# Kernel tuning notes

Measured on AMD Instinct MI355X. Metric: run time of the kernel, lower is better.

The kernel has to match this reference:

```python
import jax, jax.numpy as jnp
from jax import lax
import numpy as np

B, T, F = 64, 128, 16
H = 512
S = 2  # num_seg; SEG_DICT['2'] = [8, 6], seg_cumsum = [2, 10, 16]


def timestep_embedding(t, dim, max_period=10000.0):
    half = dim // 2
    freqs = jnp.exp(-jnp.log(max_period) * jnp.arange(half, dtype=jnp.float32) / half)
    args = t[:, None] * freqs  # [N, half]
    return jnp.concatenate([jnp.cos(args), jnp.sin(args)], axis=-1)  # [N, dim]


def setup_inputs() -> dict:
    key = jax.random.key(0)
    ks = jax.random.split(key, 16)
    sc = lambda *sh: 1.0 / np.sqrt(sh[-1])
    inp = {
        'x': jax.random.normal(ks[0], (B, T, F), dtype=jnp.float32),
        'lengths': jax.random.randint(ks[1], (B,), 1, T + 1),
        'h0': jax.random.uniform(ks[2], (B, H), dtype=jnp.float32),
        'c0': jax.random.uniform(ks[3], (B, H), dtype=jnp.float32),
        'W_is0': jax.random.normal(ks[4], (H, 8), dtype=jnp.float32) * sc(8),
        'b_is0': jax.random.normal(ks[5], (H,), dtype=jnp.float32) * 0.01,
        'W_is1': jax.random.normal(ks[6], (H, 6), dtype=jnp.float32) * sc(6),
        'b_is1': jax.random.normal(ks[7], (H,), dtype=jnp.float32) * 0.01,
        'W_ih': jax.random.normal(ks[8], (4 * H, 3 * H), dtype=jnp.float32) * sc(3 * H),
        'W_hh': jax.random.normal(ks[9], (4 * H, H), dtype=jnp.float32) * sc(H),
        'b_ih': jax.random.normal(ks[10], (4 * H,), dtype=jnp.float32) * 0.01,
        'b_hh': jax.random.normal(ks[11], (4 * H,), dtype=jnp.float32) * 0.01,
        'W_o': jax.random.normal(ks[12], (F - 2, S * H), dtype=jnp.float32) * sc(S * H),
        'b_o': jax.random.normal(ks[13], (F - 2,), dtype=jnp.float32) * 0.01,
    }
    return inp


def reference(x, lengths, h0, c0, W_is0, b_is0, W_is1, b_is1,
              W_ih, W_hh, b_ih, b_hh, W_o, b_o):
    b, t, f = x.shape
    h = h0.shape[1]
    xf = x.reshape(-1, f)  # [B*T, F]

    # timestep embeddings from the two time columns (learning_type='diff')
    tc = timestep_embedding(xf[:, 0], h)
    tp = timestep_embedding(xf[:, 1], h)
    t_emb = jnp.concatenate([tc, tp], axis=-1)  # [B*T, 2H]

    # per-segment input linears (segments = cols 2:10 and 10:16)
    e0 = xf[:, 2:10] @ W_is0.T + b_is0
    e1 = xf[:, 10:16] @ W_is1.T + b_is1
    e0 = jnp.concatenate([e0, t_emb], axis=-1)[:, None, :]  # [B*T, 1, 3H]
    e1 = jnp.concatenate([e1, t_emb], axis=-1)[:, None, :]
    # faithful to torch: concat on dim=1 then reshape(batch, num_seg, seq_len, -1)
    embs = jnp.concatenate([e0, e1], axis=1).reshape(b, S, t, 3 * h)

    def cell(carry, xt):
        hh, cc = carry
        gates = xt @ W_ih.T + b_ih + hh @ W_hh.T + b_hh
        i, fg, g, o = jnp.split(gates, 4, axis=-1)  # torch LSTMCell order i,f,g,o
        cc = jax.nn.sigmoid(fg) * cc + jax.nn.sigmoid(i) * jnp.tanh(g)
        hh = jax.nn.sigmoid(o) * jnp.tanh(cc)
        return (hh, cc), hh

    hs = []
    for s in range(S):  # shared cell weights across segments (same nn.LSTMCell object)
        xs = jnp.swapaxes(embs[:, s], 0, 1)  # [T, B, 3H]
        _, h_seq = lax.scan(cell, (h0, c0), xs)  # [T, B, H]
        hs.append(jnp.swapaxes(h_seq, 0, 1))  # [B, T, H]
    hidden_states = jnp.stack(hs, axis=-2)  # [B, T, S, H]; dropout rate 0 -> identity

    idx = lengths - 1  # final valid timestep per sequence
    hfin = hidden_states[jnp.arange(b), idx].reshape(b, S * h)  # [B, S*H]
    out = jax.nn.sigmoid(hfin @ W_o.T + b_o)  # mlp_o: Linear + Sigmoid
    return out
```

## Files before the change

### kernel.cpp

```cpp
#include <hip/hip_runtime.h>
#include <hip/hip_bf16.h>
#include <stdint.h>


typedef __attribute__((ext_vector_type(8))) short bf16x8_t;
typedef __attribute__((ext_vector_type(4))) float f32x4_t;

#define SENT 0xAAAAAAAAu

#define OFF_G      0u
#define OFF_TEMB   33554432u
#define OFF_HH     50331648u
#define OFF_WHH    67239936u
#define OFF_WMID   69337088u
#define OFF_WC0    73531392u
#define OFF_WC1    73596928u
#define OFF_BC     73662464u
#define OFF_HFIN   73678848u

__device__ __forceinline__ float bf2f(uint16_t u){
  union { uint32_t i; float f; } v; v.i = ((uint32_t)u) << 16; return v.f;
}
__device__ __forceinline__ uint16_t f2b(float f){
  union { float f; uint32_t i; } v; v.f = f;
  uint32_t r = v.i + 0x7fffu + ((v.i >> 16) & 1u);
  return (uint16_t)(r >> 16);
}
__device__ __forceinline__ float sigm(float x){ return 1.0f/(1.0f + __expf(-x)); }
__device__ __forceinline__ float tanh_(float x){
  float xc = fminf(fmaxf(x, -15.f), 15.f);
  float t = __expf(2.f*xc);
  return (t - 1.f)/(t + 1.f);
}

__global__ void prep1(const float* __restrict__ W_ih, const float* __restrict__ W_hh,
                      const float* __restrict__ W_is0, const float* __restrict__ b_is0,
                      const float* __restrict__ W_is1, const float* __restrict__ b_is1,
                      const float* __restrict__ b_ih, const float* __restrict__ b_hh,
                      uint16_t* __restrict__ whh_b, uint16_t* __restrict__ wmid_b,
                      float* __restrict__ wc0, float* __restrict__ wc1, float* __restrict__ bc){
  const int n = blockIdx.x;
  const int tid = threadIdx.x;
  __shared__ float wrow[512];
  wrow[tid]       = W_ih[(size_t)n*1536 + tid];
  wrow[tid + 256] = W_ih[(size_t)n*1536 + 256 + tid];
  for (int j = tid; j < 1024; j += 256)
    wmid_b[(size_t)n*1024 + j] = f2b(W_ih[(size_t)n*1536 + 512 + j]);
  for (int k = tid; k < 512; k += 256)
    whh_b[(size_t)n*512 + k] = f2b(W_hh[(size_t)n*512 + k]);
  __syncthreads();
  if (tid < 8){
    float s = 0.f;
    for (int k = 0; k < 512; ++k) s += wrow[k]*W_is0[k*8 + tid];
    wc0[n*8 + tid] = s;
  } else if (tid < 16){
    int c = tid - 8;
    float s = 0.f;
    if (c < 6){ for (int k = 0; k < 512; ++k) s += wrow[k]*W_is1[k*6 + c]; }
    wc1[n*8 + c] = s;
  } else if (tid == 16){
    float s = b_ih[n] + b_hh[n];
    for (int k = 0; k < 512; ++k) s += wrow[k]*b_is0[k];
    bc[n] = s;
  } else if (tid == 17){
    float s = b_ih[n] + b_hh[n];
    for (int k = 0; k < 512; ++k) s += wrow[k]*b_is1[k];
    bc[2048 + n] = s;
  }
}

__global__ void prep2(const float* __restrict__ h0, uint16_t* __restrict__ h_hist){
  int i = blockIdx.x*256 + threadIdx.x;
  uint32_t* hh = (uint32_t*)h_hist;
  if (i < 32768){
    int e    = i*2;
    int rrcg = e >> 9;
    int rr   = rrcg >> 4, cg = rrcg & 15;
    int rm   = e & 511;
    int row  = rm >> 5, u = rm & 31;
    int b    = (rr*16 + row) & 63;
    int unit = cg*32 + u;
    uint32_t lo = f2b(h0[(size_t)b*512 + unit]);
    uint32_t hi = f2b(h0[(size_t)b*512 + unit + 1]);
    uint32_t wd = lo | (hi << 16);
    if (wd == SENT) wd ^= 1u;
    hh[i] = wd;
  } else if (i < 4227072){
    hh[i] = SENT;
  }
}

__global__ void tembk(const float* __restrict__ x, uint16_t* __restrict__ temb){
  const int rid = blockIdx.x;
  const int k = threadIdx.x;
  float x0 = x[(size_t)rid*16 + 0], x1 = x[(size_t)rid*16 + 1];
  float f = __expf((float)k * (-9.210340371976184f/256.f));
  float a0 = x0*f, a1 = x1*f;
  size_t base = (size_t)rid*1024;
  temb[base + k]        = f2b(__cosf(a0));
  temb[base + 256 + k]  = f2b(__sinf(a0));
  temb[base + 512 + k]  = f2b(__cosf(a1));
  temb[base + 768 + k]  = f2b(__sinf(a1));
}

__launch_bounds__(256)
__global__ void gemmB(const uint16_t* __restrict__ temb, const uint16_t* __restrict__ wmid,
                      uint16_t* __restrict__ G){
  __shared__ __align__(16) uint16_t Al[128][72];
  __shared__ __align__(16) uint16_t Bl[128][72];
  const int tid = threadIdx.x;
  const int m0 = blockIdx.x*128, n0 = blockIdx.y*128;
  const int w = tid >> 6, lane = tid & 63;
  const int q = lane >> 4, ln = lane & 15;
  const int wm = w >> 1, wn = w & 1;
  const int srow = tid >> 1, shalf = tid & 1;

  f32x4_t acc[4][4];
  #pragma unroll
  for (int a = 0; a < 4; ++a)
    #pragma unroll
    for (int b = 0; b < 4; ++b) acc[a][b] = (f32x4_t){0.f,0.f,0.f,0.f};

  for (int kb = 0; kb < 16; ++kb){
    const uint4* ga = (const uint4*)(temb + (size_t)(m0 + srow)*1024 + kb*64 + shalf*32);
    const uint4* gb = (const uint4*)(wmid + (size_t)(n0 + srow)*1024 + kb*64 + shalf*32);
    uint4 va[4], vb[4];
    #pragma unroll
    for (int i = 0; i < 4; ++i){ va[i] = ga[i]; vb[i] = gb[i]; }
    #pragma unroll
    for (int i = 0; i < 4; ++i){
      *(uint4*)&Al[srow][shalf*32 + i*8] = va[i];
      *(uint4*)&Bl[srow][shalf*32 + i*8] = vb[i];
    }
    __syncthreads();
    #pragma unroll
    for (int kc = 0; kc < 2; ++kc){
      bf16x8_t af[4], bf[4];
      #pragma unroll
      for (int mt = 0; mt < 4; ++mt) af[mt] = *(const bf16x8_t*)&Al[wm*64 + mt*16 + ln][kc*32 + q*8];
      #pragma unroll
      for (int nt = 0; nt < 4; ++nt) bf[nt] = *(const bf16x8_t*)&Bl[wn*64 + nt*16 + ln][kc*32 + q*8];
      #pragma unroll
      for (int mt = 0; mt < 4; ++mt)
        #pragma unroll
        for (int nt = 0; nt < 4; ++nt)
          acc[mt][nt] = __builtin_amdgcn_mfma_f32_16x16x32_bf16(af[mt], bf[nt], acc[mt][nt], 0, 0, 0);
    }
    __syncthreads();
  }
  #pragma unroll
  for (int mt = 0; mt < 4; ++mt)
    #pragma unroll
    for (int nt = 0; nt < 4; ++nt)
      #pragma unroll
      for (int r = 0; r < 4; ++r){
        int Mr = m0 + wm*64 + mt*16 + q*4 + r;
        int Nc = n0 + wn*64 + nt*16 + ln;
        G[(size_t)Mr*2048 + Nc] = f2b(acc[mt][nt][r]);
      }
}

__launch_bounds__(256)
__global__ void lstmk(const float* __restrict__ x, const float* __restrict__ c0,
                      const int* __restrict__ lengths,
                      const uint16_t* __restrict__ whh_b, const uint16_t* __restrict__ G,
                      const float* __restrict__ wc0, const float* __restrict__ wc1,
                      const float* __restrict__ bc,
                      uint16_t* __restrict__ h_hist, float* __restrict__ hfin){
  __shared__ __align__(16) uint16_t h_l[2][16][552];

  const int tid = threadIdx.x;
  const int bid = blockIdx.x;
  const int rr = bid & 7;
  const int g  = bid >> 3;
  const int k0 = g*32;
  const int sp = rr >> 2;
  const int w = tid >> 6, lane = tid & 63;
  const int q = lane >> 4, ln = lane & 15;
  const int u8 = ln & 7, gh = ln >> 3;
  const int unit = k0 + w*8 + u8;
  const int gl0 = gh*512 + unit;
  const int gl1 = (2 + gh)*512 + unit;

  const int LVL = 65536;

  bf16x8_t barr0[16], barr1[16];
  #pragma unroll
  for (int kc = 0; kc < 16; ++kc){
    barr0[kc] = *(const bf16x8_t*)(whh_b + (size_t)gl0*512 + kc*32 + q*8);
    barr1[kc] = *(const bf16x8_t*)(whh_b + (size_t)gl1*512 + kc*32 + q*8);
  }
  bf16x8_t e0f[2], e1f[2];
  #pragma unroll
  for (int nsI = 0; nsI < 2; ++nsI){
    bf16x8_t v0 = {0,0,0,0,0,0,0,0}, v1 = {0,0,0,0,0,0,0,0};
    if (q == 0){
      const float* wcs = nsI ? wc1 : wc0;
      #pragma unroll
      for (int jj = 0; jj < 8; ++jj){
        ((uint16_t*)&v0)[jj] = f2b(wcs[gl0*8 + jj]);
        ((uint16_t*)&v1)[jj] = f2b(wcs[gl1*8 + jj]);
      }
    }
    e0f[nsI] = v0; e1f[nsI] = v1;
  }
  float bc0v[2] = { bc[gl0], bc[2048 + gl0] };
  float bc1v[2] = { bc[gl1], bc[2048 + gl1] };

  int   bmr[4], lenr[4];
  float cst[4];
  #pragma unroll
  for (int r = 0; r < 4; ++r){
    int row = rr*16 + q*4 + r;
    bmr[r]  = row & 63;
    lenr[r] = lengths[bmr[r]];
    cst[r]  = c0[(size_t)bmr[r]*512 + unit];
  }

  const int prow = lane >> 2;
  const int pcol = (lane & 3)*8;
  const int xm = tid >> 3, xc = tid & 7;
  const int xb = (rr*16 + xm) & 63;

  const size_t stb = ((size_t)rr*8192 + g*512);

  for (int idx = tid; idx < 2*16*32; idx += 256)
    h_l[idx >> 9][(idx >> 5) & 15][520 + (idx & 31)] = 0;

  for (int t = 0; t < 128; ++t){
    const int qidx = sp*128 + t;
    const int ntm = qidx >> 1;
    const int ns  = qidx & 1;
    const int buf = t & 1;

    uint16_t g0r[4], g1r[4];
    #pragma unroll
    for (int r = 0; r < 4; ++r){
      size_t grow = (size_t)(bmr[r]*128 + ntm)*2048;
      g0r[r] = G[grow + gl0];
      g1r[r] = G[grow + gl1];
    }
    float xv = 0.f;
    if (tid < 128){
      if (ns == 0)      xv = x[(size_t)(xb*128 + ntm)*16 + 2 + xc];
      else if (xc < 6)  xv = x[(size_t)(xb*128 + ntm)*16 + 10 + xc];
    }

    {
      const unsigned long long* lvl = (const unsigned long long*)h_hist
                                      + (((size_t)t*LVL + (size_t)rr*8192) >> 2);
      unsigned long long hv[4][2];
      while (true){
        bool ok = true;
        #pragma unroll
        for (int i = 0; i < 4; ++i){
          const unsigned long long* p = lvl + ((size_t)(w*4 + i)*128 + prow*8 + (pcol >> 2));
          hv[i][0] = __hip_atomic_load(&p[0], __ATOMIC_RELAXED, __HIP_MEMORY_SCOPE_AGENT);
          hv[i][1] = __hip_atomic_load(&p[1], __ATOMIC_RELAXED, __HIP_MEMORY_SCOPE_AGENT);
          ok &= ((uint32_t)hv[i][0] != SENT) & ((uint32_t)(hv[i][0] >> 32) != SENT)
              & ((uint32_t)hv[i][1] != SENT) & ((uint32_t)(hv[i][1] >> 32) != SENT);
        }
        if (__all(ok)) break;
        __builtin_amdgcn_s_sleep(1);
      }
      #pragma unroll
      for (int i = 0; i < 4; ++i){
        int reg = w*4 + i;
        *(unsigned long long*)&h_l[buf][prow][reg*32 + pcol]     = hv[i][0];
        *(unsigned long long*)&h_l[buf][prow][reg*32 + pcol + 4] = hv[i][1];
      }
    }
    if (tid < 128) h_l[buf][xm][512 + xc] = f2b(xv);
    __syncthreads();

    f32x4_t acc0, acc1;
    {
      float b0 = ns ? bc0v[1] : bc0v[0];
      float b1 = ns ? bc1v[1] : bc1v[0];
      #pragma unroll
      for (int r = 0; r < 4; ++r){ acc0[r] = bf2f(g0r[r]) + b0; acc1[r] = bf2f(g1r[r]) + b1; }
    }
    #pragma unroll
    for (int kc = 0; kc < 16; ++kc){
      bf16x8_t a = *(const bf16x8_t*)&h_l[buf][ln][kc*32 + q*8];
      acc0 = __builtin_amdgcn_mfma_f32_16x16x32_bf16(a, barr0[kc], acc0, 0, 0, 0);
      acc1 = __builtin_amdgcn_mfma_f32_16x16x32_bf16(a, barr1[kc], acc1, 0, 0, 0);
    }
    {
      bf16x8_t a = *(const bf16x8_t*)&h_l[buf][ln][512 + q*8];
      acc0 = __builtin_amdgcn_mfma_f32_16x16x32_bf16(a, ns ? e0f[1] : e0f[0], acc0, 0, 0, 0);
      acc1 = __builtin_amdgcn_mfma_f32_16x16x32_bf16(a, ns ? e1f[1] : e1f[0], acc1, 0, 0, 0);
    }

    float pf[4], po[4];
    #pragma unroll
    for (int r = 0; r < 4; ++r){
      pf[r] = __shfl_xor(acc0[r], 8);
      po[r] = __shfl_xor(acc1[r], 8);
    }
    if (ln < 8){
      uint32_t hb[4]; float hF[4];
      #pragma unroll
      for (int r = 0; r < 4; ++r){
        float ig = acc0[r], fg = pf[r], gg = acc1[r], og = po[r];
        cst[r] = sigm(fg)*cst[r] + sigm(ig)*tanh_(gg);
        float h = sigm(og)*tanh_(cst[r]);
        hF[r] = h; hb[r] = (uint32_t)f2b(h);
      }
      #pragma unroll
      for (int r = 0; r < 4; ++r){
        uint32_t ph = (uint32_t)__shfl_xor((int)hb[r], 1);
        uint32_t packed = hb[r] | (ph << 16);
        if (packed == SENT) packed ^= 1u;
        uint32_t hi = (uint32_t)__shfl_xor((int)packed, 2);
        if ((ln & 3) == 0){
          unsigned long long v = (unsigned long long)packed | ((unsigned long long)hi << 32);
          unsigned long long* hp = (unsigned long long*)h_hist
              + (((size_t)(t+1)*LVL + stb + (size_t)(q*4 + r)*32 + w*8 + u8) >> 2);
          __hip_atomic_store(hp, v, __ATOMIC_RELAXED, __HIP_MEMORY_SCOPE_AGENT);
        }
        if (t == lenr[r] - 1)
          hfin[(size_t)bmr[r]*1024 + sp*512 + unit] = hF[r];
      }
    }
  }
}

__global__ void outk(const float* __restrict__ hfin, const float* __restrict__ W_o,
                     const float* __restrict__ b_o, float* __restrict__ out){
  __shared__ float hl[1024];
  __shared__ float red[16][17];
  const int b = blockIdx.x, tid = threadIdx.x;
  #pragma unroll
  for (int i = 0; i < 4; ++i) hl[tid + i*256] = hfin[(size_t)b*1024 + tid + i*256];
  __syncthreads();
  const int o = tid >> 4, j0 = tid & 15;
  float s = 0.f;
  if (o < 14){
    for (int j = j0; j < 1024; j += 16) s += hl[j]*W_o[(size_t)o*1024 + j];
  }
  red[o][j0] = s;
  __syncthreads();
  if (tid < 14){
    float tot = b_o[tid];
    #pragma unroll
    for (int i = 0; i < 16; ++i) tot += red[tid][i];
    out[b*14 + tid] = 1.0f/(1.0f + __expf(-tot));
  }
}

extern "C" void kernel_launch(void* const* d_in, const int* in_sizes, int n_in,
                              void* d_out, int out_size, void* d_ws, size_t ws_size,
                              hipStream_t stream){
  const float* x     = (const float*)d_in[0];
  const int*   lens  = (const int*)  d_in[1];
  const float* h0    = (const float*)d_in[2];
  const float* c0    = (const float*)d_in[3];
  const float* W_is0 = (const float*)d_in[4];
  const float* b_is0 = (const float*)d_in[5];
  const float* W_is1 = (const float*)d_in[6];
  const float* b_is1 = (const float*)d_in[7];
  const float* W_ih  = (const float*)d_in[8];
  const float* W_hh  = (const float*)d_in[9];
  const float* b_ih  = (const float*)d_in[10];
  const float* b_hh  = (const float*)d_in[11];
  const float* W_o   = (const float*)d_in[12];
  const float* b_o   = (const float*)d_in[13];
  float* out = (float*)d_out;

  char* ws = (char*)d_ws;
  uint16_t* G      = (uint16_t*)(ws + OFF_G);
  uint16_t* temb   = (uint16_t*)(ws + OFF_TEMB);
  uint16_t* h_hist = (uint16_t*)(ws + OFF_HH);
  uint16_t* whh_b  = (uint16_t*)(ws + OFF_WHH);
  uint16_t* wmid_b = (uint16_t*)(ws + OFF_WMID);
  float* wc0  = (float*)(ws + OFF_WC0);
  float* wc1  = (float*)(ws + OFF_WC1);
  float* bc   = (float*)(ws + OFF_BC);
  float* hfin = (float*)(ws + OFF_HFIN);

  hipLaunchKernelGGL(prep1, dim3(2048), dim3(256), 0, stream,
                     W_ih, W_hh, W_is0, b_is0, W_is1, b_is1, b_ih, b_hh,
                     whh_b, wmid_b, wc0, wc1, bc);
  hipLaunchKernelGGL(prep2, dim3(16512), dim3(256), 0, stream, h0, h_hist);
  hipLaunchKernelGGL(tembk, dim3(8192), dim3(256), 0, stream, x, temb);
  hipLaunchKernelGGL(gemmB, dim3(64, 16), dim3(256), 0, stream, temb, wmid_b, G);
  hipLaunchKernelGGL(lstmk, dim3(128), dim3(256), 0, stream,
                     x, c0, lens, whh_b, G, wc0, wc1, bc, h_hist, hfin);
  hipLaunchKernelGGL(outk, dim3(64), dim3(256), 0, stream, hfin, W_o, b_o, out);
}
```

Measured before the change: 600.0 us.

## Add fast-path hidden-state exchange buffer with sc0 polling before agent-scope fallback

Adds a second hidden-state history buffer that reuses the temb workspace after gemmB has consumed it. Each step now polls this buffer a bounded number of times using inline-asm sc0 vector loads, and falls back to the original agent-scope atomic polling if the data has not appeared. Producers write h to both buffers. The aim is to cut inter-block synchronization latency in the sequential LSTM recurrence, at the cost of extra stores and a larger sentinel-initialization kernel. The fast-path stores use workgroup scope across blocks, which weakens the memory-ordering guarantees the exchange relies on.

```diff
diff --git a/kernel.cpp b/kernel.cpp
--- a/kernel.cpp
+++ b/kernel.cpp
@@ -5,8 +5,10 @@
 
 typedef __attribute__((ext_vector_type(8))) short bf16x8_t;
 typedef __attribute__((ext_vector_type(4))) float f32x4_t;
+typedef __attribute__((ext_vector_type(4))) unsigned int u32x4_t;
 
 #define SENT 0xAAAAAAAAu
+#define FAST_TRIES 10
 
 #define OFF_G      0u
 #define OFF_TEMB   33554432u
@@ -69,9 +71,11 @@
   }
 }
 
-__global__ void prep2(const float* __restrict__ h0, uint16_t* __restrict__ h_hist){
+__global__ void prep2(const float* __restrict__ h0, uint16_t* __restrict__ h_hist,
+                      uint16_t* __restrict__ h_fast){
   int i = blockIdx.x*256 + threadIdx.x;
   uint32_t* hh = (uint32_t*)h_hist;
+  uint32_t* hf = (uint32_t*)h_fast;
   if (i < 32768){
     int e    = i*2;
     int rrcg = e >> 9;
@@ -87,6 +91,8 @@
     hh[i] = wd;
   } else if (i < 4227072){
     hh[i] = SENT;
+  } else if (i < 8421376){
+    hf[i - 4227072] = SENT;
   }
 }
 
@@ -166,7 +172,8 @@
                       const uint16_t* __restrict__ whh_b, const uint16_t* __restrict__ G,
                       const float* __restrict__ wc0, const float* __restrict__ wc1,
                       const float* __restrict__ bc,
-                      uint16_t* __restrict__ h_hist, float* __restrict__ hfin){
+                      uint16_t* __restrict__ h_hist, uint16_t* __restrict__ h_fast,
+                      float* __restrict__ hfin){
   __shared__ __align__(16) uint16_t h_l[2][16][552];
 
   const int tid = threadIdx.x;
@@ -246,29 +253,59 @@
       else if (xc < 6)  xv = x[(size_t)(xb*128 + ntm)*16 + 10 + xc];
     }
 
-    {
-      const unsigned long long* lvl = (const unsigned long long*)h_hist
-                                      + (((size_t)t*LVL + (size_t)rr*8192) >> 2);
-      unsigned long long hv[4][2];
+    u32x4_t hv4[4];
+    bool got = false;
+    if (t > 0){
+      const uint16_t* fl = h_fast + (size_t)(t-1)*LVL + (size_t)rr*8192;
+      const u32x4_t* p0 = (const u32x4_t*)(fl + (size_t)(w*4 + 0)*512 + prow*32 + pcol);
+      const u32x4_t* p1 = (const u32x4_t*)(fl + (size_t)(w*4 + 1)*512 + prow*32 + pcol);
+      const u32x4_t* p2 = (const u32x4_t*)(fl + (size_t)(w*4 + 2)*512 + prow*32 + pcol);
+      const u32x4_t* p3 = (const u32x4_t*)(fl + (size_t)(w*4 + 3)*512 + prow*32 + pcol);
+      for (int it = 0; it < FAST_TRIES; ++it){
+        u32x4_t a, b, c, d;
+        asm volatile(
+          "global_load_dwordx4 %0, %4, off sc0\n\t"
+          "global_load_dwordx4 %1, %5, off sc0\n\t"
+          "global_load_dwordx4 %2, %6, off sc0\n\t"
+          "global_load_dwordx4 %3, %7, off sc0\n\t"
+          "s_waitcnt vmcnt(0)"
+          : "=&v"(a), "=&v"(b), "=&v"(c), "=&v"(d)
+          : "v"(p0), "v"(p1), "v"(p2), "v"(p3)
+          : "memory");
+        hv4[0] = a; hv4[1] = b; hv4[2] = c; hv4[3] = d;
+        bool ok = true;
+        #pragma unroll
+        for (int i = 0; i < 4; ++i)
+          #pragma unroll
+          for (int jx = 0; jx < 4; ++jx)
+            ok &= (hv4[i][jx] != SENT);
+        if (__all(ok)){ got = true; break; }
+        __builtin_amdgcn_s_sleep(1);
+      }
+    }
+    if (!got){
+      const unsigned long long* lvl = (const unsigned long long*)
+          (h_hist + (size_t)t*LVL + (size_t)rr*8192);
       while (true){
         bool ok = true;
         #pragma unroll
         for (int i = 0; i < 4; ++i){
           const unsigned long long* p = lvl + ((size_t)(w*4 + i)*128 + prow*8 + (pcol >> 2));
-          hv[i][0] = __hip_atomic_load(&p[0], __ATOMIC_RELAXED, __HIP_MEMORY_SCOPE_AGENT);
-          hv[i][1] = __hip_atomic_load(&p[1], __ATOMIC_RELAXED, __HIP_MEMORY_SCOPE_AGENT);
-          ok &= ((uint32_t)hv[i][0] != SENT) & ((uint32_t)(hv[i][0] >> 32) != SENT)
-              & ((uint32_t)hv[i][1] != SENT) & ((uint32_t)(hv[i][1] >> 32) != SENT);
+          unsigned long long a = __hip_atomic_load(&p[0], __ATOMIC_RELAXED, __HIP_MEMORY_SCOPE_AGENT);
+          unsigned long long b = __hip_atomic_load(&p[1], __ATOMIC_RELAXED, __HIP_MEMORY_SCOPE_AGENT);
+          hv4[i][0] = (uint32_t)a; hv4[i][1] = (uint32_t)(a >> 32);
+          hv4[i][2] = (uint32_t)b; hv4[i][3] = (uint32_t)(b >> 32);
+          ok &= (hv4[i][0] != SENT) & (hv4[i][1] != SENT)
+              & (hv4[i][2] != SENT) & (hv4[i][3] != SENT);
         }
         if (__all(ok)) break;
         __builtin_amdgcn_s_sleep(1);
       }
-      #pragma unroll
-      for (int i = 0; i < 4; ++i){
-        int reg = w*4 + i;
-        *(unsigned long long*)&h_l[buf][prow][reg*32 + pcol]     = hv[i][0];
-        *(unsigned long long*)&h_l[buf][prow][reg*32 + pcol + 4] = hv[i][1];
-      }
+    }
+    #pragma unroll
+    for (int i = 0; i < 4; ++i){
+      int reg = w*4 + i;
+      *(u32x4_t*)&h_l[buf][prow][reg*32 + pcol] = hv4[i];
     }
     if (tid < 128) h_l[buf][xm][512 + xc] = f2b(xv);
     __syncthreads();
@@ -315,9 +352,11 @@
         uint32_t hi = (uint32_t)__shfl_xor((int)packed, 2);
         if ((ln & 3) == 0){
           unsigned long long v = (unsigned long long)packed | ((unsigned long long)hi << 32);
-          unsigned long long* hp = (unsigned long long*)h_hist
-              + (((size_t)(t+1)*LVL + stb + (size_t)(q*4 + r)*32 + w*8 + u8) >> 2);
+          size_t eoff = stb + (size_t)(q*4 + r)*32 + w*8 + u8;
+          unsigned long long* hp = (unsigned long long*)(h_hist + (size_t)(t+1)*LVL + eoff);
           __hip_atomic_store(hp, v, __ATOMIC_RELAXED, __HIP_MEMORY_SCOPE_AGENT);
+          unsigned long long* fp = (unsigned long long*)(h_fast + (size_t)t*LVL + eoff);
+          __hip_atomic_store(fp, v, __ATOMIC_RELAXED, __HIP_MEMORY_SCOPE_WORKGROUP);
         }
         if (t == lenr[r] - 1)
           hfin[(size_t)bmr[r]*1024 + sp*512 + unit] = hF[r];
@@ -378,14 +417,15 @@
   float* wc1  = (float*)(ws + OFF_WC1);
   float* bc   = (float*)(ws + OFF_BC);
   float* hfin = (float*)(ws + OFF_HFIN);
+  uint16_t* h_fast = temb;
 
   hipLaunchKernelGGL(prep1, dim3(2048), dim3(256), 0, stream,
                      W_ih, W_hh, W_is0, b_is0, W_is1, b_is1, b_ih, b_hh,
                      whh_b, wmid_b, wc0, wc1, bc);
-  hipLaunchKernelGGL(prep2, dim3(16512), dim3(256), 0, stream, h0, h_hist);
   hipLaunchKernelGGL(tembk, dim3(8192), dim3(256), 0, stream, x, temb);
   hipLaunchKernelGGL(gemmB, dim3(64, 16), dim3(256), 0, stream, temb, wmid_b, G);
+  hipLaunchKernelGGL(prep2, dim3(32896), dim3(256), 0, stream, h0, h_hist, h_fast);
   hipLaunchKernelGGL(lstmk, dim3(128), dim3(256), 0, stream,
-                     x, c0, lens, whh_b, G, wc0, wc1, bc, h_hist, hfin);
+                     x, c0, lens, whh_b, G, wc0, wc1, bc, h_hist, h_fast, hfin);
   hipLaunchKernelGGL(outk, dim3(64), dim3(256), 0, stream, hfin, W_o, b_o, out);
 }
```

Result: slower. 875.9 us (+46.0%).

## Use direct global-to-LDS loads and staged epilogue in gemmB; parallelize prep1 reductions

Applied to the files above, without the earlier changes.

gemmB now fills shared-memory tiles with global_load_lds 16-byte transfers instead of register round-trips. The unpadded layout may add LDS bank conflicts on the fragment reads. Its epilogue stages the bf16 results through shared memory so rows are written to global memory with coalesced 16-byte stores instead of scattered 2-byte stores. prep1 spreads the small dot-product reductions over all 256 threads with a shared-memory partial-sum stage, replacing 18 serial threads.

```diff
diff --git a/kernel.cpp b/kernel.cpp
--- a/kernel.cpp
+++ b/kernel.cpp
@@ -32,6 +32,11 @@
   float t = __expf(2.f*xc);
   return (t - 1.f)/(t + 1.f);
 }
+__device__ __forceinline__ void gl_lds16(const void* g, void* l){
+  __builtin_amdgcn_global_load_lds(
+      (const __attribute__((address_space(1))) void*)g,
+      (__attribute__((address_space(3))) void*)l, 16, 0, 0);
+}
 
 __global__ void prep1(const float* __restrict__ W_ih, const float* __restrict__ W_hh,
                       const float* __restrict__ W_is0, const float* __restrict__ b_is0,
@@ -42,6 +47,7 @@
   const int n = blockIdx.x;
   const int tid = threadIdx.x;
   __shared__ float wrow[512];
+  __shared__ float red[16][17];
   wrow[tid]       = W_ih[(size_t)n*1536 + tid];
   wrow[tid + 256] = W_ih[(size_t)n*1536 + 256 + tid];
   for (int j = tid; j < 1024; j += 256)
@@ -49,23 +55,33 @@
   for (int k = tid; k < 512; k += 256)
     whh_b[(size_t)n*512 + k] = f2b(W_hh[(size_t)n*512 + k]);
   __syncthreads();
-  if (tid < 8){
+  {
+    const int d = tid >> 4, jp = tid & 15;
     float s = 0.f;
-    for (int k = 0; k < 512; ++k) s += wrow[k]*W_is0[k*8 + tid];
-    wc0[n*8 + tid] = s;
-  } else if (tid < 16){
-    int c = tid - 8;
-    float s = 0.f;
-    if (c < 6){ for (int k = 0; k < 512; ++k) s += wrow[k]*W_is1[k*6 + c]; }
-    wc1[n*8 + c] = s;
+    const int kk0 = jp*32;
+    if (d < 8){
+      for (int k = kk0; k < kk0 + 32; ++k) s += wrow[k]*W_is0[k*8 + d];
+    } else if (d < 14){
+      int c = d - 8;
+      for (int k = kk0; k < kk0 + 32; ++k) s += wrow[k]*W_is1[k*6 + c];
+    } else if (d == 14){
+      for (int k = kk0; k < kk0 + 32; ++k) s += wrow[k]*b_is0[k];
+    } else {
+      for (int k = kk0; k < kk0 + 32; ++k) s += wrow[k]*b_is1[k];
+    }
+    red[d][jp] = s;
+  }
+  __syncthreads();
+  if (tid < 16){
+    float tot = 0.f;
+    #pragma unroll
+    for (int i = 0; i < 16; ++i) tot += red[tid][i];
+    if (tid < 8)       wc0[n*8 + tid] = tot;
+    else if (tid < 14) wc1[n*8 + (tid - 8)] = tot;
+    else if (tid == 14) bc[n]        = b_ih[n] + b_hh[n] + tot;
+    else                bc[2048 + n] = b_ih[n] + b_hh[n] + tot;
   } else if (tid == 16){
-    float s = b_ih[n] + b_hh[n];
-    for (int k = 0; k < 512; ++k) s += wrow[k]*b_is0[k];
-    bc[n] = s;
-  } else if (tid == 17){
-    float s = b_ih[n] + b_hh[n];
-    for (int k = 0; k < 512; ++k) s += wrow[k]*b_is1[k];
-    bc[2048 + n] = s;
+    wc1[n*8 + 6] = 0.f; wc1[n*8 + 7] = 0.f;
   }
 }
 
@@ -106,14 +122,16 @@
 __launch_bounds__(256)
 __global__ void gemmB(const uint16_t* __restrict__ temb, const uint16_t* __restrict__ wmid,
                       uint16_t* __restrict__ G){
-  __shared__ __align__(16) uint16_t Al[128][72];
-  __shared__ __align__(16) uint16_t Bl[128][72];
+  __shared__ __align__(16) uint16_t smem[16384];
+  uint16_t* Al = smem;
+  uint16_t* Bl = smem + 8192;
   const int tid = threadIdx.x;
   const int m0 = blockIdx.x*128, n0 = blockIdx.y*128;
   const int w = tid >> 6, lane = tid & 63;
   const int q = lane >> 4, ln = lane & 15;
   const int wm = w >> 1, wn = w & 1;
-  const int srow = tid >> 1, shalf = tid & 1;
+  const int srow_l = (lane >> 3);
+  const int scol   = (lane & 7)*8;
 
   f32x4_t acc[4][4];
   #pragma unroll
@@ -122,24 +140,23 @@
     for (int b = 0; b < 4; ++b) acc[a][b] = (f32x4_t){0.f,0.f,0.f,0.f};
 
   for (int kb = 0; kb < 16; ++kb){
-    const uint4* ga = (const uint4*)(temb + (size_t)(m0 + srow)*1024 + kb*64 + shalf*32);
-    const uint4* gb = (const uint4*)(wmid + (size_t)(n0 + srow)*1024 + kb*64 + shalf*32);
-    uint4 va[4], vb[4];
-    #pragma unroll
-    for (int i = 0; i < 4; ++i){ va[i] = ga[i]; vb[i] = gb[i]; }
     #pragma unroll
     for (int i = 0; i < 4; ++i){
-      *(uint4*)&Al[srow][shalf*32 + i*8] = va[i];
-      *(uint4*)&Bl[srow][shalf*32 + i*8] = vb[i];
+      int row0 = w*32 + i*8;
+      int row  = row0 + srow_l;
+      gl_lds16(temb + (size_t)(m0 + row)*1024 + kb*64 + scol, &Al[row0*64]);
+      gl_lds16(wmid + (size_t)(n0 + row)*1024 + kb*64 + scol, &Bl[row0*64]);
     }
     __syncthreads();
     #pragma unroll
     for (int kc = 0; kc < 2; ++kc){
       bf16x8_t af[4], bf[4];
       #pragma unroll
-      for (int mt = 0; mt < 4; ++mt) af[mt] = *(const bf16x8_t*)&Al[wm*64 + mt*16 + ln][kc*32 + q*8];
-      #pragma unroll
-      for (int nt = 0; nt < 4; ++nt) bf[nt] = *(const bf16x8_t*)&Bl[wn*64 + nt*16 + ln][kc*32 + q*8];
+      for (int mt = 0; mt < 4; ++mt)
+        af[mt] = *(const bf16x8_t*)&Al[(wm*64 + mt*16 + ln)*64 + kc*32 + q*8];
+      #pragma unroll
+      for (int nt = 0; nt < 4; ++nt)
+        bf[nt] = *(const bf16x8_t*)&Bl[(wn*64 + nt*16 + ln)*64 + kc*32 + q*8];
       #pragma unroll
       for (int mt = 0; mt < 4; ++mt)
         #pragma unroll
@@ -148,16 +165,25 @@
     }
     __syncthreads();
   }
+
   #pragma unroll
   for (int mt = 0; mt < 4; ++mt)
     #pragma unroll
     for (int nt = 0; nt < 4; ++nt)
       #pragma unroll
       for (int r = 0; r < 4; ++r){
-        int Mr = m0 + wm*64 + mt*16 + q*4 + r;
-        int Nc = n0 + wn*64 + nt*16 + ln;
-        G[(size_t)Mr*2048 + Nc] = f2b(acc[mt][nt][r]);
-      }
+        int Mr = wm*64 + mt*16 + q*4 + r;
+        int Nc = wn*64 + nt*16 + ln;
+        smem[Mr*128 + Nc] = f2b(acc[mt][nt][r]);
+      }
+  __syncthreads();
+  {
+    const int erow = tid >> 1, eh = tid & 1;
+    uint4* gdst = (uint4*)(G + (size_t)(m0 + erow)*2048 + n0 + eh*64);
+    const uint4* lsrc = (const uint4*)&smem[erow*128 + eh*64];
+    #pragma unroll
+    for (int i2 = 0; i2 < 8; ++i2) gdst[i2] = lsrc[i2];
+  }
 }
 
 __launch_bounds__(256)
```

Measured after the change: 590.4 us. No clear change (-1.6%).
